# Kernel optimization log

Hardware: AMD Instinct MI355X
Metric: run time of the kernel (lower is better)

Reference implementation:

```python
import jax, jax.numpy as jnp
import numpy as np

D_MODEL = 1024
N_HEADS = 16
HEAD_DIM = D_MODEL // N_HEADS
N_EXPERTS = 4
HIDDEN = 4 * D_MODEL
B, T = 1, 2048


def _apply_rope(x, sin, cos):
    # x: [..., D]; sin/cos broadcastable to [..., D/2]
    x1, x2 = x[..., ::2], x[..., 1::2]
    r1 = x1 * cos - x2 * sin
    r2 = x1 * sin + x2 * cos
    return jnp.stack((r1, r2), axis=-1).reshape(x.shape)


def setup_inputs() -> dict:
    key = jax.random.key(0)
    ks = jax.random.split(key, 16)
    s = 0.02
    d, E, Hd = D_MODEL, N_EXPERTS, HIDDEN
    return {
        "x": jax.random.normal(ks[0], (B, T, d), dtype=jnp.float32),
        "w_dw": jax.random.normal(ks[1], (d, 3), dtype=jnp.float32) * s,      # depthwise conv k=3
        "w_pw": jax.random.normal(ks[2], (d, d), dtype=jnp.float32) * s,      # pointwise conv [out,in]
        "w_qkv": jax.random.normal(ks[3], (3 * d, d), dtype=jnp.float32) * s,  # [out,in]
        "w_o": jax.random.normal(ks[4], (d, d), dtype=jnp.float32) * s,
        "w_gate": jax.random.normal(ks[5], (d, d), dtype=jnp.float32) * s,
        "b_gate": jnp.zeros((d,), dtype=jnp.float32),
        "ln_g": jnp.ones((d,), dtype=jnp.float32),
        "ln_b": jnp.zeros((d,), dtype=jnp.float32),
        "w_moe_gate": jax.random.normal(ks[6], (E, d), dtype=jnp.float32) * s,  # Linear no bias [out,in]
        "w1": jax.random.normal(ks[7], (E, Hd, d), dtype=jnp.float32) * s,
        "b1": jnp.zeros((E, Hd), dtype=jnp.float32),
        "w2": jax.random.normal(ks[8], (E, d, Hd), dtype=jnp.float32) * s,
        "b2": jnp.zeros((E, d), dtype=jnp.float32),
    }


def reference(x, w_dw, w_pw, w_qkv, w_o, w_gate, b_gate, ln_g, ln_b,
              w_moe_gate, w1, b1, w2, b2):
    Bv, Tv, d = x.shape
    H, Dh = N_HEADS, HEAD_DIM
    dt = x.dtype

    # --- causal conv mixer (depthwise k=3, causal left pad 2, then pointwise) ---
    xp = jnp.pad(x, ((0, 0), (2, 0), (0, 0)))
    y = (xp[:, 0:Tv] * w_dw[:, 0] + xp[:, 1:Tv + 1] * w_dw[:, 1]
         + xp[:, 2:Tv + 2] * w_dw[:, 2])
    y = jnp.einsum('btd,ed->bte', y, w_pw)
    x = x + y

    # --- qkv projection + split heads ---
    qkv = jnp.einsum('btd,ed->bte', x, w_qkv).reshape(Bv, Tv, 3, H, Dh)
    q, k, v = qkv[:, :, 0], qkv[:, :, 1], qkv[:, :, 2]

    # --- RoPE (head_dim even) ---
    inv_freq = 1.0 / (10000.0 ** (jnp.arange(0, Dh, 2, dtype=dt) / Dh))
    pos = jnp.arange(Tv, dtype=dt)
    theta = pos[:, None] * inv_freq[None, :]                 # [T, Dh/2]
    sin = jnp.sin(theta)[None, :, None, :]                   # [1,T,1,Dh/2]
    cos = jnp.cos(theta)[None, :, None, :]
    q = _apply_rope(q, sin, cos)
    k = _apply_rope(k, sin, cos)

    # --- linear attention via full kv outer-product cumsum ---
    q_phi = jax.nn.elu(q) + 1.0
    k_phi = jax.nn.elu(k) + 1.0
    kv = k_phi[..., :, None] * v[..., None, :]               # [B,T,H,D,D]
    kv_prefix = jnp.cumsum(kv, axis=1)
    k_prefix = jnp.cumsum(k_phi, axis=1)
    num = jnp.einsum('bthd,bthdm->bthm', q_phi, kv_prefix)
    denom = jnp.sum(q_phi * k_prefix, axis=-1, keepdims=True)
    attn = num / (denom + 1e-6)
    attn = attn.reshape(Bv, Tv, d)
    attn = jnp.einsum('btd,ed->bte', attn, w_o)

    # --- delta-gated residual (dropout = identity in eval) ---
    delta = x - jnp.concatenate([x[:, :1], x[:, :-1]], axis=1)
    gate = jax.nn.sigmoid(jnp.einsum('btd,ed->bte', delta, w_gate) + b_gate)
    x = x + gate * attn

    # --- LayerNorm + dense MoE FFN ---
    mu = jnp.mean(x, axis=-1, keepdims=True)
    var = jnp.mean((x - mu) ** 2, axis=-1, keepdims=True)
    h = (x - mu) / jnp.sqrt(var + 1e-5) * ln_g + ln_b

    gw = jax.nn.softmax(jnp.einsum('btd,ed->bte', h, w_moe_gate), axis=-1)  # [B,T,E]
    hid = jax.nn.silu(jnp.einsum('btd,efd->btef', h, w1) + b1)              # [B,T,E,Hd]
    eo = jnp.einsum('btef,edf->bted', hid, w2) + b2                          # [B,T,E,d]
    ffn = jnp.einsum('bte,bted->btd', gw, eo)
    return x + ffn
```

## Files before the change

### kernel.cpp

```cpp
#include <hip/hip_runtime.h>
#include <hip/hip_bf16.h>

#define TSEQ 2048
#define DM   1024
#define NHD  16
#define DHD  64
#define NEXP 4
#define HIDN 4096
#define NMOE (NEXP*HIDN)
#define CHK  128
#define NCHK (TSEQ/CHK)

typedef __attribute__((ext_vector_type(8))) short          bf16x8_v;
typedef __attribute__((ext_vector_type(4))) float          f32x4_v;
typedef __attribute__((ext_vector_type(4))) unsigned short us4_v;

__device__ __forceinline__ unsigned short bfbits(float f) {
  __hip_bfloat16 h = __float2bfloat16(f);
  return __builtin_bit_cast(unsigned short, h);
}
__device__ __forceinline__ float bf2f(unsigned short u) {
  return __uint_as_float(((unsigned)u) << 16);
}
__device__ __forceinline__ float wave_sum(float v) {
  #pragma unroll
  for (int o = 32; o; o >>= 1) v += __shfl_xor(v, o, 64);
  return v;
}
__device__ __forceinline__ void gl_lds16(const void* g, void* l) {
  __builtin_amdgcn_global_load_lds((const __attribute__((address_space(1))) void*)g,
                                   (__attribute__((address_space(3))) void*)l, 16, 0, 0);
}

__global__ __launch_bounds__(256) void cvt_bf16(const float* __restrict__ in,
                                                unsigned short* __restrict__ out, int n4) {
  int i = blockIdx.x * 256 + threadIdx.x;
  if (i >= n4) return;
  float4 v = ((const float4*)in)[i];
  us4_v o; o.x = bfbits(v.x); o.y = bfbits(v.y); o.z = bfbits(v.z); o.w = bfbits(v.w);
  ((us4_v*)out)[i] = o;
}

__global__ __launch_bounds__(256) void perm_w2(const float* __restrict__ in,
                                               unsigned short* __restrict__ out) {
  int i = blockIdx.x * 256 + threadIdx.x;
  int i4 = i * 4;
  int f = i4 & (HIDN - 1);
  int r = i4 >> 12;
  int e = r >> 10, dd = r & 1023;
  float4 v = *(const float4*)&in[(size_t)r * HIDN + f];
  us4_v o; o.x = bfbits(v.x); o.y = bfbits(v.y); o.z = bfbits(v.z); o.w = bfbits(v.w);
  *(us4_v*)&out[(size_t)dd * NMOE + e * HIDN + f] = o;
}

__global__ __launch_bounds__(256) void conv_dw(const float* __restrict__ x,
                                               const float* __restrict__ w_dw,
                                               unsigned short* __restrict__ y_bf) {
  int i = blockIdx.x * 256 + threadIdx.x;
  int c = i & (DM - 1);
  int t = i >> 10;
  float a = (t >= 2) ? x[i - 2 * DM] : 0.f;
  float b = (t >= 1) ? x[i - DM]     : 0.f;
  float d = x[i];
  float y = a * w_dw[c * 3] + b * w_dw[c * 3 + 1] + d * w_dw[c * 3 + 2];
  y_bf[i] = bfbits(y);
}

template <int EPI>
__global__ __launch_bounds__(256) void gemm_bt(
    const unsigned short* __restrict__ A,  const unsigned short* __restrict__ A2,
    const unsigned short* __restrict__ B,  const unsigned short* __restrict__ B2,
    float* __restrict__ Cf, float* __restrict__ Cf2,
    unsigned short* __restrict__ Cbf,
    const float* __restrict__ ex0,
    int lda, int ldb, int K, int ldc)
{
  if (EPI == 0) { if (blockIdx.z) { A = A2; B = B2; Cf = Cf2; } }

  __shared__ unsigned short As[2][128][32];
  __shared__ unsigned short Bs[2][128][32];

  const int tid = threadIdx.x;
  const int m0 = blockIdx.x << 7, n0 = blockIdx.y << 7;
  const int sr = tid >> 2, sc = (tid & 3) << 3;
  const unsigned short* gA = A + (size_t)(m0 + sr) * lda + sc;
  const unsigned short* gB = B + (size_t)(n0 + sr) * ldb + sc;

  const int lane = tid & 63, wv = tid >> 6;
  const int wr = (wv >> 1) << 6, wc = (wv & 1) << 6;
  const int fr = lane & 15, fk = (lane >> 4) << 3, r4 = (lane >> 4) << 2;

  f32x4_v acc[4][4] = {};

  auto stage = [&](int k0, int b) {
    gl_lds16(gA + k0,                     &As[b][sr][sc]);
    gl_lds16(gA + k0 + (size_t)64 * lda,  &As[b][sr + 64][sc]);
    gl_lds16(gB + k0,                     &Bs[b][sr][sc]);
    gl_lds16(gB + k0 + (size_t)64 * ldb,  &Bs[b][sr + 64][sc]);
  };

  stage(0, 0);
  __syncthreads();
  int cur = 0;
  for (int k0 = 0; k0 < K; k0 += 32) {
    if (k0 + 32 < K) stage(k0 + 32, cur ^ 1);
    bf16x8_v af[4], bfm[4];
    #pragma unroll
    for (int m = 0; m < 4; m++) af[m]  = *(const bf16x8_v*)&As[cur][wr + m * 16 + fr][fk];
    #pragma unroll
    for (int n = 0; n < 4; n++) bfm[n] = *(const bf16x8_v*)&Bs[cur][wc + n * 16 + fr][fk];
    #pragma unroll
    for (int m = 0; m < 4; m++)
      #pragma unroll
      for (int n = 0; n < 4; n++)
        acc[m][n] = __builtin_amdgcn_mfma_f32_16x16x32_bf16(af[m], bfm[n], acc[m][n], 0, 0, 0);
    __syncthreads();
    cur ^= 1;
  }

  #pragma unroll
  for (int m = 0; m < 4; m++) {
    #pragma unroll
    for (int n = 0; n < 4; n++) {
      #pragma unroll
      for (int j = 0; j < 4; j++) {
        int gr = m0 + wr + m * 16 + r4 + j;
        int gc = n0 + wc + n * 16 + fr;
        float v = acc[m][n][j];
        size_t off = (size_t)gr * ldc + gc;
        if (EPI == 0) {
          Cf[off] = v;
        } else {
          float s = v + ex0[off];
          Cf[off] = s; Cbf[off] = bfbits(s);
        }
      }
    }
  }
}

template <int EPI>
__global__ __launch_bounds__(512, 1) void gemm256(
    const unsigned short* __restrict__ A, const unsigned short* __restrict__ B,
    float* __restrict__ Cf, unsigned short* __restrict__ Cbf,
    const float* __restrict__ ex0, const float* __restrict__ ex1,
    int lda, int ldb, int K, int ldc, int kPerZ)
{
  if (EPI == 1) { int ko = blockIdx.z * kPerZ; A += ko; B += ko; K = kPerZ; }

  __shared__ unsigned short As[2][256][64];
  __shared__ unsigned short Bs[2][256][64];

  int bidl = blockIdx.y * gridDim.x + blockIdx.x;
  int chunk = (gridDim.x * gridDim.y) >> 3;
  int swz = (bidl & 7) * chunk + (bidl >> 3);
  int m0 = (swz & 7) << 8, n0 = (swz >> 3) << 8;

  const int tid = threadIdx.x;
  const int srow = tid >> 3;
  const int scol = (tid & 7) << 3;
  const int scsw = (((tid & 7) ^ ((tid >> 3) & 7)) << 3);
  const unsigned short* gA = A + (size_t)(m0 + srow) * lda + scsw;
  const unsigned short* gB = B + (size_t)(n0 + srow) * ldb + scsw;

  auto stageA = [&](int k0, int b) {
    #pragma unroll
    for (int i = 0; i < 4; i++)
      gl_lds16(gA + (size_t)(i * 64) * lda + k0, &As[b][i * 64 + srow][scol]);
  };
  auto stageB = [&](int k0, int b) {
    #pragma unroll
    for (int i = 0; i < 4; i++)
      gl_lds16(gB + (size_t)(i * 64) * ldb + k0, &Bs[b][i * 64 + srow][scol]);
  };

  const int lane = tid & 63, wv = tid >> 6;
  const int wm = wv >> 2, wn = wv & 3;
  const int fr = lane & 15;
  const int kreg = lane >> 4, r4 = kreg << 2;
  const int c0 = ((kreg) ^ (lane & 7)) << 3;
  const int c1 = ((4 + kreg) ^ (lane & 7)) << 3;

  f32x4_v acc[8][4] = {};
  bf16x8_v a0[4][2], a1[4][2], bb[2][2];

  stageA(0, 0); stageB(0, 0);
  const int nt = K >> 6;
  for (int t = 0; t < nt; t++) {
    const int p = t & 1;
    if (t + 1 < nt) {
      stageA((t + 1) << 6, p ^ 1);
      asm volatile("s_waitcnt vmcnt(4)" ::: "memory");
    } else {
      asm volatile("s_waitcnt vmcnt(0)" ::: "memory");
    }
    __builtin_amdgcn_s_barrier();
    #pragma unroll
    for (int m = 0; m < 4; m++) {
      a0[m][0] = *(const bf16x8_v*)&As[p][wm * 128 + m * 16 + fr][c0];
      a0[m][1] = *(const bf16x8_v*)&As[p][wm * 128 + m * 16 + fr][c1];
    }
    #pragma unroll
    for (int n = 0; n < 2; n++) {
      bb[n][0] = *(const bf16x8_v*)&Bs[p][wn * 64 + n * 16 + fr][c0];
      bb[n][1] = *(const bf16x8_v*)&Bs[p][wn * 64 + n * 16 + fr][c1];
    }
    __builtin_amdgcn_s_setprio(1);
    #pragma unroll
    for (int m = 0; m < 4; m++)
      #pragma unroll
      for (int n = 0; n < 2; n++) {
        acc[m][n] = __builtin_amdgcn_mfma_f32_16x16x32_bf16(a0[m][0], bb[n][0], acc[m][n], 0, 0, 0);
        acc[m][n] = __builtin_amdgcn_mfma_f32_16x16x32_bf16(a0[m][1], bb[n][1], acc[m][n], 0, 0, 0);
      }
    __builtin_amdgcn_s_setprio(0);
    __builtin_amdgcn_s_barrier();
    #pragma unroll
    for (int m = 0; m < 4; m++) {
      a1[m][0] = *(const bf16x8_v*)&As[p][wm * 128 + 64 + m * 16 + fr][c0];
      a1[m][1] = *(const bf16x8_v*)&As[p][wm * 128 + 64 + m * 16 + fr][c1];
    }
    __builtin_amdgcn_s_setprio(1);
    #pragma unroll
    for (int m = 0; m < 4; m++)
      #pragma unroll
      for (int n = 0; n < 2; n++) {
        acc[m + 4][n] = __builtin_amdgcn_mfma_f32_16x16x32_bf16(a1[m][0], bb[n][0], acc[m + 4][n], 0, 0, 0);
        acc[m + 4][n] = __builtin_amdgcn_mfma_f32_16x16x32_bf16(a1[m][1], bb[n][1], acc[m + 4][n], 0, 0, 0);
      }
    __builtin_amdgcn_s_setprio(0);
    __builtin_amdgcn_s_barrier();
    #pragma unroll
    for (int n = 0; n < 2; n++) {
      bb[n][0] = *(const bf16x8_v*)&Bs[p][wn * 64 + 32 + n * 16 + fr][c0];
      bb[n][1] = *(const bf16x8_v*)&Bs[p][wn * 64 + 32 + n * 16 + fr][c1];
    }
    if (t + 1 < nt) stageB((t + 1) << 6, p ^ 1);
    __builtin_amdgcn_s_setprio(1);
    #pragma unroll
    for (int m = 0; m < 4; m++)
      #pragma unroll
      for (int n = 0; n < 2; n++) {
        acc[m][n + 2] = __builtin_amdgcn_mfma_f32_16x16x32_bf16(a0[m][0], bb[n][0], acc[m][n + 2], 0, 0, 0);
        acc[m][n + 2] = __builtin_amdgcn_mfma_f32_16x16x32_bf16(a0[m][1], bb[n][1], acc[m][n + 2], 0, 0, 0);
      }
    __builtin_amdgcn_s_setprio(0);
    __builtin_amdgcn_s_barrier();
    __builtin_amdgcn_s_setprio(1);
    #pragma unroll
    for (int m = 0; m < 4; m++)
      #pragma unroll
      for (int n = 0; n < 2; n++) {
        acc[m + 4][n + 2] = __builtin_amdgcn_mfma_f32_16x16x32_bf16(a1[m][0], bb[n][0], acc[m + 4][n + 2], 0, 0, 0);
        acc[m + 4][n + 2] = __builtin_amdgcn_mfma_f32_16x16x32_bf16(a1[m][1], bb[n][1], acc[m + 4][n + 2], 0, 0, 0);
      }
    __builtin_amdgcn_s_setprio(0);
    __builtin_amdgcn_s_barrier();
  }

  #pragma unroll
  for (int m = 0; m < 8; m++)
    #pragma unroll
    for (int n = 0; n < 4; n++)
      #pragma unroll
      for (int j = 0; j < 4; j++) {
        int grow = m0 + wm * 128 + m * 16 + r4 + j;
        int gcol = n0 + wn * 64 + n * 16 + fr;
        size_t off = (size_t)grow * ldc + gcol;
        if (EPI == 0) {
          float c2 = acc[m][n][j] + ex0[gcol];
          float sl = c2 / (1.f + __expf(-c2));
          Cbf[off] = bfbits(sl * ex1[grow * 4 + (gcol >> 12)]);
        } else {
          atomicAdd(&Cf[off], acc[m][n][j]);
        }
      }
}

__global__ __launch_bounds__(256) void rope_phi(const float* __restrict__ qkv,
                                                unsigned short* __restrict__ qphi,
                                                unsigned short* __restrict__ kphi,
                                                unsigned short* __restrict__ vout) {
  int idx = blockIdx.x * 256 + threadIdx.x;
  int i = idx & 31;
  int h = (idx >> 5) & 15;
  int t = idx >> 9;
  const float* row = qkv + (size_t)t * 3 * DM;
  int col = h * 64 + 2 * i;
  float q0 = row[col],          q1 = row[col + 1];
  float k0 = row[DM + col],     k1 = row[DM + col + 1];
  float v0 = row[2 * DM + col], v1 = row[2 * DM + col + 1];
  float invf = __expf(-(float)(2 * i) * (9.210340371976184f / 64.f));
  float th = (float)t * invf;
  float s, c;
  sincosf(th, &s, &c);
  float qr0 = q0 * c - q1 * s, qr1 = q0 * s + q1 * c;
  float kr0 = k0 * c - k1 * s, kr1 = k0 * s + k1 * c;
  size_t o = (size_t)t * DM + col;
  qphi[o]     = bfbits(qr0 > 0.f ? qr0 + 1.f : __expf(qr0));
  qphi[o + 1] = bfbits(qr1 > 0.f ? qr1 + 1.f : __expf(qr1));
  kphi[o]     = bfbits(kr0 > 0.f ? kr0 + 1.f : __expf(kr0));
  kphi[o + 1] = bfbits(kr1 > 0.f ? kr1 + 1.f : __expf(kr1));
  vout[o]     = bfbits(v0);
  vout[o + 1] = bfbits(v1);
}

__global__ __launch_bounds__(256) void kv_chunk(const unsigned short* __restrict__ kphi,
                                                const unsigned short* __restrict__ vbf,
                                                float* __restrict__ kvT,
                                                float* __restrict__ ksbuf) {
  int h = blockIdx.x & 15, c = blockIdx.x >> 4;
  __shared__ unsigned short Kt[64][136];
  __shared__ unsigned short Vt[64][136];
  int tid = threadIdx.x;
  int rr = tid >> 3, cc = (tid & 7) << 3;
  int t0 = c * CHK;
  #pragma unroll
  for (int g = 0; g < 4; g++) {
    int t = g * 32 + rr;
    bf16x8_v k8 = *(const bf16x8_v*)&kphi[(size_t)(t0 + t) * DM + h * 64 + cc];
    bf16x8_v v8 = *(const bf16x8_v*)&vbf [(size_t)(t0 + t) * DM + h * 64 + cc];
    #pragma unroll
    for (int j = 0; j < 8; j++) { Kt[cc + j][t] = (unsigned short)k8[j];
                                  Vt[cc + j][t] = (unsigned short)v8[j]; }
  }
  __syncthreads();
  int lane = tid & 63, wv = tid >> 6;
  int wr = (wv >> 1) << 5, wc = (wv & 1) << 5;
  int fr = lane & 15, fk = (lane >> 4) << 3, r4 = (lane >> 4) << 2;
  f32x4_v acc[2][2] = {};
  #pragma unroll
  for (int k0 = 0; k0 < 128; k0 += 32) {
    bf16x8_v a[2], b[2];
    #pragma unroll
    for (int m = 0; m < 2; m++) a[m] = *(const bf16x8_v*)&Kt[wr + m * 16 + fr][k0 + fk];
    #pragma unroll
    for (int n = 0; n < 2; n++) b[n] = *(const bf16x8_v*)&Vt[wc + n * 16 + fr][k0 + fk];
    #pragma unroll
    for (int m = 0; m < 2; m++)
      #pragma unroll
      for (int n = 0; n < 2; n++)
        acc[m][n] = __builtin_amdgcn_mfma_f32_16x16x32_bf16(a[m], b[n], acc[m][n], 0, 0, 0);
  }
  float* kvout = kvT + (size_t)(h * NCHK + c) * 4096;
  #pragma unroll
  for (int m = 0; m < 2; m++)
    #pragma unroll
    for (int n = 0; n < 2; n++)
      #pragma unroll
      for (int j = 0; j < 4; j++)
        kvout[(wc + n * 16 + fr) * 64 + (wr + m * 16 + r4 + j)] = acc[m][n][j];
  float s = 0.f;
  int d = tid >> 2, q = tid & 3;
  for (int i = 0; i < 32; i++) s += bf2f(Kt[d][q * 32 + i]);
  s += __shfl_xor(s, 1, 64); s += __shfl_xor(s, 2, 64);
  if (q == 0) ksbuf[(h * NCHK + c) * 64 + d] = s;
}

__global__ __launch_bounds__(256) void prefix_kv(const float* __restrict__ kvT,
                                                 const float* __restrict__ ksbuf,
                                                 unsigned short* __restrict__ sT,
                                                 float* __restrict__ kspre) {
  int idx = blockIdx.x * 256 + threadIdx.x;
  int h = idx >> 12, nd = idx & 4095;
  float s = 0.f;
  for (int c = 0; c < NCHK; c++) {
    size_t o = (size_t)(h * NCHK + c) * 4096 + nd;
    sT[o] = bfbits(s);
    s += kvT[o];
  }
  if (idx < NHD * 64) {
    float ks = 0.f;
    for (int c = 0; c < NCHK; c++) {
      int o = ((idx >> 6) * NCHK + c) * 64 + (idx & 63);
      kspre[o] = ks;
      ks += ksbuf[o];
    }
  }
}

__global__ __launch_bounds__(256) void attn_chunk(const unsigned short* __restrict__ qphi,
                                                  const unsigned short* __restrict__ kphi,
                                                  const unsigned short* __restrict__ vbf,
                                                  const unsigned short* __restrict__ sT,
                                                  const float* __restrict__ kspre,
                                                  float* __restrict__ num,
                                                  float* __restrict__ den) {
  int h = blockIdx.x & 15, c = blockIdx.x >> 4;
  __shared__ unsigned short Qs[128][72];
  __shared__ unsigned short Ks[128][72];
  __shared__ unsigned short Ms[128][200];
  __shared__ unsigned short Vt[64][200];
  __shared__ float ksL[64];
  int tid = threadIdx.x;
  int t0 = c * CHK;
  int rr = tid >> 3, cc = (tid & 7) << 3;
  #pragma unroll
  for (int g = 0; g < 4; g++) {
    int t = g * 32 + rr;
    bf16x8_v q8 = *(const bf16x8_v*)&qphi[(size_t)(t0 + t) * DM + h * 64 + cc];
    bf16x8_v k8 = *(const bf16x8_v*)&kphi[(size_t)(t0 + t) * DM + h * 64 + cc];
    bf16x8_v v8 = *(const bf16x8_v*)&vbf [(size_t)(t0 + t) * DM + h * 64 + cc];
    *(bf16x8_v*)&Qs[t][cc] = q8;
    *(bf16x8_v*)&Ks[t][cc] = k8;
    *(bf16x8_v*)&Ms[t][128 + cc] = q8;
    #pragma unroll
    for (int j = 0; j < 8; j++) Vt[cc + j][t] = (unsigned short)v8[j];
  }
  #pragma unroll
  for (int g = 0; g < 2; g++) {
    int e = (g * 256 + tid) * 8;
    bf16x8_v s8 = *(const bf16x8_v*)&sT[(size_t)(h * NCHK + c) * 4096 + e];
    *(bf16x8_v*)&Vt[e >> 6][128 + (e & 63)] = s8;
  }
  if (tid < 64) ksL[tid] = kspre[(h * NCHK + c) * 64 + tid];
  __syncthreads();

  int lane = tid & 63, wv = tid >> 6;
  int wr = (wv >> 1) << 6, wc = (wv & 1) << 6;
  int fr = lane & 15, fk = (lane >> 4) << 3, r4 = (lane >> 4) << 2;
  {
    f32x4_v acc[4][4] = {};
    #pragma unroll
    for (int k0 = 0; k0 < 64; k0 += 32) {
      bf16x8_v a[4], b[4];
      #pragma unroll
      for (int m = 0; m < 4; m++) a[m] = *(const bf16x8_v*)&Qs[wr + m * 16 + fr][k0 + fk];
      #pragma unroll
      for (int n = 0; n < 4; n++) b[n] = *(const bf16x8_v*)&Ks[wc + n * 16 + fr][k0 + fk];
      #pragma unroll
      for (int m = 0; m < 4; m++)
        #pragma unroll
        for (int n = 0; n < 4; n++)
          acc[m][n] = __builtin_amdgcn_mfma_f32_16x16x32_bf16(a[m], b[n], acc[m][n], 0, 0, 0);
    }
    #pragma unroll
    for (int m = 0; m < 4; m++)
      #pragma unroll
      for (int n = 0; n < 4; n++)
        #pragma unroll
        for (int j = 0; j < 4; j++) {
          int r = wr + m * 16 + r4 + j, col = wc + n * 16 + fr;
          Ms[r][col] = bfbits(col <= r ? acc[m][n][j] : 0.f);
        }
  }
  __syncthreads();
  {
    int dr = tid >> 1, half = tid & 1;
    float s = 0.f;
    for (int i = 0; i < 64; i++) s += bf2f(Ms[dr][half * 64 + i]);
    for (int i = 0; i < 32; i++) {
      int d = half * 32 + i;
      s += bf2f(Qs[dr][d]) * ksL[d];
    }
    s += __shfl_xor(s, 1, 64);
    if (!half) den[(size_t)(t0 + dr) * NHD + h] = s;
  }
  {
    int wc2 = (wv & 1) << 5;
    f32x4_v acc[4][2] = {};
    #pragma unroll
    for (int k0 = 0; k0 < 192; k0 += 32) {
      bf16x8_v a[4], b[2];
      #pragma unroll
      for (int m = 0; m < 4; m++) a[m] = *(const bf16x8_v*)&Ms[wr + m * 16 + fr][k0 + fk];
      #pragma unroll
      for (int n = 0; n < 2; n++) b[n] = *(const bf16x8_v*)&Vt[wc2 + n * 16 + fr][k0 + fk];
      #pragma unroll
      for (int m = 0; m < 4; m++)
        #pragma unroll
        for (int n = 0; n < 2; n++)
          acc[m][n] = __builtin_amdgcn_mfma_f32_16x16x32_bf16(a[m], b[n], acc[m][n], 0, 0, 0);
    }
    #pragma unroll
    for (int m = 0; m < 4; m++)
      #pragma unroll
      for (int n = 0; n < 2; n++)
        #pragma unroll
        for (int j = 0; j < 4; j++)
          num[(size_t)(t0 + wr + m * 16 + r4 + j) * DM + h * 64 + wc2 + n * 16 + fr]
              = acc[m][n][j];
  }
}

__global__ __launch_bounds__(256) void div_cvt(const float* __restrict__ attn_num,
                                               const float* __restrict__ denom,
                                               const float* __restrict__ x1,
                                               unsigned short* __restrict__ attn_bf,
                                               unsigned short* __restrict__ delta_bf) {
  int i = blockIdx.x * 256 + threadIdx.x;
  int i4 = i * 4;
  int t = i4 >> 10, c = i4 & 1023, h = c >> 6;
  float dn = 1.f / (denom[t * NHD + h] + 1e-6f);
  float4 nm = *(const float4*)&attn_num[i4];
  us4_v a; a.x = bfbits(nm.x * dn); a.y = bfbits(nm.y * dn);
           a.z = bfbits(nm.z * dn); a.w = bfbits(nm.w * dn);
  *(us4_v*)&attn_bf[i4] = a;
  float4 xv = *(const float4*)&x1[i4];
  float4 xp = t ? *(const float4*)&x1[i4 - DM] : xv;
  us4_v d; d.x = bfbits(xv.x - xp.x); d.y = bfbits(xv.y - xp.y);
           d.z = bfbits(xv.z - xp.z); d.w = bfbits(xv.w - xp.w);
  *(us4_v*)&delta_bf[i4] = d;
}

__global__ __launch_bounds__(256) void fuse_ln(const float* __restrict__ x1,
                                               const float* __restrict__ attn_o,
                                               const float* __restrict__ gate_lin,
                                               const float* __restrict__ b_gate,
                                               const float* __restrict__ ln_g,
                                               const float* __restrict__ ln_b,
                                               const float* __restrict__ w_moe,
                                               float* __restrict__ x2,
                                               unsigned short* __restrict__ h_bf,
                                               float* __restrict__ gw) {
  int t = blockIdx.x;
  int tid = threadIdx.x;
  __shared__ float hrow[DM];
  __shared__ float red[16];
  float vals[4], s = 0.f, s2 = 0.f;
  #pragma unroll
  for (int j = 0; j < 4; j++) {
    int c = tid + j * 256;
    size_t ix = (size_t)t * DM + c;
    float g = gate_lin[ix] + b_gate[c];
    float sig = 1.f / (1.f + __expf(-g));
    float xv = x1[ix] + sig * attn_o[ix];
    x2[ix] = xv; vals[j] = xv; s += xv; s2 += xv * xv;
  }
  s = wave_sum(s); s2 = wave_sum(s2);
  int wvi = tid >> 6, l = tid & 63;
  if (l == 0) { red[wvi] = s; red[4 + wvi] = s2; }
  __syncthreads();
  s  = red[0] + red[1] + red[2] + red[3];
  s2 = red[4] + red[5] + red[6] + red[7];
  float mu = s * (1.f / DM);
  float var = s2 * (1.f / DM) - mu * mu;
  float rstd = rsqrtf(var + 1e-5f);
  #pragma unroll
  for (int j = 0; j < 4; j++) {
    int c = tid + j * 256;
    size_t ix = (size_t)t * DM + c;
    float h = (vals[j] - mu) * rstd * ln_g[c] + ln_b[c];
    h_bf[ix] = bfbits(h); hrow[c] = h;
  }
  __syncthreads();
  float dot = 0.f;
  for (int i0 = l; i0 < DM; i0 += 64) dot += hrow[i0] * w_moe[wvi * DM + i0];
  dot = wave_sum(dot);
  if (l == 0) red[8 + wvi] = dot;
  __syncthreads();
  if (tid == 0) {
    float a0 = red[8], a1 = red[9], a2 = red[10], a3 = red[11];
    float mx = fmaxf(fmaxf(a0, a1), fmaxf(a2, a3));
    float e0 = __expf(a0 - mx), e1 = __expf(a1 - mx), e2 = __expf(a2 - mx), e3 = __expf(a3 - mx);
    float inv = 1.f / (e0 + e1 + e2 + e3);
    gw[t * 4 + 0] = e0 * inv; gw[t * 4 + 1] = e1 * inv;
    gw[t * 4 + 2] = e2 * inv; gw[t * 4 + 3] = e3 * inv;
  }
}

__global__ __launch_bounds__(256) void init_out(const float* __restrict__ x2,
                                                const float* __restrict__ gw,
                                                const float* __restrict__ b2,
                                                float* __restrict__ out) {
  int i = blockIdx.x * 256 + threadIdx.x;
  int i4 = i * 4;
  int t = i4 >> 10, c = i4 & 1023;
  const float* g = gw + t * 4;
  float4 o = *(const float4*)&x2[i4];
  #pragma unroll
  for (int e = 0; e < 4; e++) {
    float ge = g[e];
    float4 b = *(const float4*)&b2[e * DM + c];
    o.x += ge * b.x; o.y += ge * b.y; o.z += ge * b.z; o.w += ge * b.w;
  }
  *(float4*)&out[i4] = o;
}

extern "C" void kernel_launch(void* const* d_in, const int* in_sizes, int n_in,
                              void* d_out, int out_size, void* d_ws, size_t ws_size,
                              hipStream_t stream) {
  const float* x      = (const float*)d_in[0];
  const float* w_dw   = (const float*)d_in[1];
  const float* w_pw   = (const float*)d_in[2];
  const float* w_qkv  = (const float*)d_in[3];
  const float* w_o    = (const float*)d_in[4];
  const float* w_gate = (const float*)d_in[5];
  const float* b_gate = (const float*)d_in[6];
  const float* ln_g   = (const float*)d_in[7];
  const float* ln_b   = (const float*)d_in[8];
  const float* w_moe  = (const float*)d_in[9];
  const float* w1     = (const float*)d_in[10];
  const float* b1     = (const float*)d_in[11];
  const float* w2     = (const float*)d_in[12];
  const float* b2     = (const float*)d_in[13];
  float* out = (float*)d_out;

  char* ws = (char*)d_ws;
  size_t off = 0;
  auto alloc = [&](size_t bytes) -> char* {
    char* p = ws + off; off += (bytes + 255) & ~(size_t)255; return p;
  };
  unsigned short* w_pw_bf   = (unsigned short*)alloc((size_t)DM * DM * 2);
  unsigned short* w_qkv_bf  = (unsigned short*)alloc((size_t)3 * DM * DM * 2);
  unsigned short* w_o_bf    = (unsigned short*)alloc((size_t)DM * DM * 2);
  unsigned short* w_gate_bf = (unsigned short*)alloc((size_t)DM * DM * 2);
  unsigned short* w1_bf     = (unsigned short*)alloc((size_t)NMOE * DM * 2);
  unsigned short* w2c_bf    = (unsigned short*)alloc((size_t)DM * NMOE * 2);
  float*          x1        = (float*)alloc((size_t)TSEQ * DM * 4);
  unsigned short* x1_bf     = (unsigned short*)alloc((size_t)TSEQ * DM * 2);
  unsigned short* y_bf      = (unsigned short*)alloc((size_t)TSEQ * DM * 2);
  float*          denomb    = (float*)alloc((size_t)TSEQ * NHD * 4);
  float*          gwb       = (float*)alloc((size_t)TSEQ * NEXP * 4);
  float*          attn_o    = (float*)alloc((size_t)TSEQ * DM * 4);
  unsigned short* delta_bf  = (unsigned short*)alloc((size_t)TSEQ * DM * 2);
  float*          gate_lin  = (float*)alloc((size_t)TSEQ * DM * 4);
  float*          x2        = (float*)alloc((size_t)TSEQ * DM * 4);
  unsigned short* h_bf      = (unsigned short*)alloc((size_t)TSEQ * DM * 2);
  float*          kvT       = (float*)alloc((size_t)NHD * NCHK * 4096 * 4);
  unsigned short* sTb       = (unsigned short*)alloc((size_t)NHD * NCHK * 4096 * 2);
  float*          ksbuf     = (float*)alloc((size_t)NHD * NCHK * 64 * 4);
  float*          kspre     = (float*)alloc((size_t)NHD * NCHK * 64 * 4);
  char*           pool      = alloc((size_t)TSEQ * NMOE * 2);
  if (off > ws_size) return;

  float*          qkv      = (float*)pool;
  unsigned short* qphi     = (unsigned short*)(pool + (size_t)TSEQ * 3 * DM * 4);
  unsigned short* kphi     = qphi + (size_t)TSEQ * DM;
  unsigned short* vbf      = kphi + (size_t)TSEQ * DM;
  float*          attn_num = (float*)(vbf + (size_t)TSEQ * DM);
  unsigned short* attn_bf  = (unsigned short*)(attn_num + (size_t)TSEQ * DM);
  unsigned short* hids     = (unsigned short*)pool;

  cvt_bf16<<<1024,  256, 0, stream>>>(w_pw,   w_pw_bf,   DM * DM / 4);
  cvt_bf16<<<3072,  256, 0, stream>>>(w_qkv,  w_qkv_bf,  3 * DM * DM / 4);
  cvt_bf16<<<1024,  256, 0, stream>>>(w_o,    w_o_bf,    DM * DM / 4);
  cvt_bf16<<<1024,  256, 0, stream>>>(w_gate, w_gate_bf, DM * DM / 4);
  cvt_bf16<<<16384, 256, 0, stream>>>(w1,     w1_bf,     NMOE * DM / 4);
  perm_w2<<<16384, 256, 0, stream>>>(w2, w2c_bf);

  conv_dw<<<8192, 256, 0, stream>>>(x, w_dw, y_bf);
  gemm_bt<1><<<dim3(16, 8, 1), 256, 0, stream>>>(y_bf, nullptr, w_pw_bf, nullptr,
      x1, nullptr, x1_bf, x, DM, DM, DM, DM);

  gemm_bt<0><<<dim3(16, 24, 1), 256, 0, stream>>>(x1_bf, nullptr, w_qkv_bf, nullptr,
      qkv, nullptr, nullptr, nullptr, DM, DM, DM, 3 * DM);
  rope_phi<<<4096, 256, 0, stream>>>(qkv, qphi, kphi, vbf);

  kv_chunk<<<NHD * NCHK, 256, 0, stream>>>(kphi, vbf, kvT, ksbuf);
  prefix_kv<<<256, 256, 0, stream>>>(kvT, ksbuf, sTb, kspre);
  attn_chunk<<<NHD * NCHK, 256, 0, stream>>>(qphi, kphi, vbf, sTb, kspre,
                                             attn_num, denomb);
  div_cvt<<<2048, 256, 0, stream>>>(attn_num, denomb, x1, attn_bf, delta_bf);

  gemm_bt<0><<<dim3(16, 8, 2), 256, 0, stream>>>(attn_bf, delta_bf, w_o_bf, w_gate_bf,
      attn_o, gate_lin, nullptr, nullptr, DM, DM, DM, DM);

  fuse_ln<<<2048, 256, 0, stream>>>(x1, attn_o, gate_lin, b_gate, ln_g, ln_b, w_moe,
                                    x2, h_bf, gwb);

  init_out<<<2048, 256, 0, stream>>>(x2, gwb, b2, out);
  gemm256<0><<<dim3(8, 64, 1), 512, 0, stream>>>(h_bf, w1_bf, nullptr, hids,
      b1, gwb, DM, DM, DM, NMOE, 0);
  gemm256<1><<<dim3(8, 4, 8), 512, 0, stream>>>(hids, w2c_bf, out, nullptr,
      nullptr, nullptr, NMOE, NMOE, NMOE, DM, NMOE / 8);
}
```

Measured before the change: 387.9 us.

## Rework small GEMMs, fuse attention normalization, drop w2 permute, trim barriers

```diff
diff --git a/kernel.cpp b/kernel.cpp
--- a/kernel.cpp
+++ b/kernel.cpp
@@ -39,18 +39,6 @@
   float4 v = ((const float4*)in)[i];
   us4_v o; o.x = bfbits(v.x); o.y = bfbits(v.y); o.z = bfbits(v.z); o.w = bfbits(v.w);
   ((us4_v*)out)[i] = o;
-}
-
-__global__ __launch_bounds__(256) void perm_w2(const float* __restrict__ in,
-                                               unsigned short* __restrict__ out) {
-  int i = blockIdx.x * 256 + threadIdx.x;
-  int i4 = i * 4;
-  int f = i4 & (HIDN - 1);
-  int r = i4 >> 12;
-  int e = r >> 10, dd = r & 1023;
-  float4 v = *(const float4*)&in[(size_t)r * HIDN + f];
-  us4_v o; o.x = bfbits(v.x); o.y = bfbits(v.y); o.z = bfbits(v.z); o.w = bfbits(v.w);
-  *(us4_v*)&out[(size_t)dd * NMOE + e * HIDN + f] = o;
 }
 
 __global__ __launch_bounds__(256) void conv_dw(const float* __restrict__ x,
@@ -67,76 +55,102 @@
 }
 
 template <int EPI>
-__global__ __launch_bounds__(256) void gemm_bt(
-    const unsigned short* __restrict__ A,  const unsigned short* __restrict__ A2,
-    const unsigned short* __restrict__ B,  const unsigned short* __restrict__ B2,
+__global__ __launch_bounds__(256, 2) void gemm128s(
+    const unsigned short* __restrict__ A, const unsigned short* __restrict__ A2,
+    const unsigned short* __restrict__ B, const unsigned short* __restrict__ B2,
     float* __restrict__ Cf, float* __restrict__ Cf2,
-    unsigned short* __restrict__ Cbf,
-    const float* __restrict__ ex0,
+    unsigned short* __restrict__ Cbf, const float* __restrict__ ex0,
     int lda, int ldb, int K, int ldc)
 {
   if (EPI == 0) { if (blockIdx.z) { A = A2; B = B2; Cf = Cf2; } }
 
-  __shared__ unsigned short As[2][128][32];
-  __shared__ unsigned short Bs[2][128][32];
+  __shared__ unsigned short As[2][128][64];
+  __shared__ unsigned short Bs[2][128][64];
+
+  const int nwg = gridDim.x * gridDim.y;
+  const int bidl = blockIdx.y * gridDim.x + blockIdx.x;
+  const int chunk = nwg >> 3;
+  const int swz = (bidl & 7) * chunk + (bidl >> 3);
+  const int ntn = gridDim.y;
+  const int rest = swz >> 3;
+  const int m0 = ((rest / ntn) * 8 + (swz & 7)) << 7;
+  const int n0 = (rest % ntn) << 7;
 
   const int tid = threadIdx.x;
-  const int m0 = blockIdx.x << 7, n0 = blockIdx.y << 7;
-  const int sr = tid >> 2, sc = (tid & 3) << 3;
-  const unsigned short* gA = A + (size_t)(m0 + sr) * lda + sc;
-  const unsigned short* gB = B + (size_t)(n0 + sr) * ldb + sc;
+  const int srow = tid >> 3;
+  const int scol = (tid & 7) << 3;
+  const int scsw = (((tid & 7) ^ ((tid >> 3) & 7)) << 3);
+  const unsigned short* gA = A + (size_t)(m0 + srow) * lda + scsw;
+  const unsigned short* gB = B + (size_t)(n0 + srow) * ldb + scsw;
+
+  auto stage = [&](int k0, int b) {
+    #pragma unroll
+    for (int i = 0; i < 4; i++)
+      gl_lds16(gA + (size_t)(i * 32) * lda + k0, &As[b][i * 32 + srow][scol]);
+    #pragma unroll
+    for (int i = 0; i < 4; i++)
+      gl_lds16(gB + (size_t)(i * 32) * ldb + k0, &Bs[b][i * 32 + srow][scol]);
+  };
 
   const int lane = tid & 63, wv = tid >> 6;
   const int wr = (wv >> 1) << 6, wc = (wv & 1) << 6;
-  const int fr = lane & 15, fk = (lane >> 4) << 3, r4 = (lane >> 4) << 2;
+  const int fr = lane & 15, kreg = lane >> 4, r4 = kreg << 2;
+  const int c0 = ((kreg) ^ (lane & 7)) << 3;
+  const int c1 = ((4 + kreg) ^ (lane & 7)) << 3;
 
   f32x4_v acc[4][4] = {};
 
-  auto stage = [&](int k0, int b) {
-    gl_lds16(gA + k0,                     &As[b][sr][sc]);
-    gl_lds16(gA + k0 + (size_t)64 * lda,  &As[b][sr + 64][sc]);
-    gl_lds16(gB + k0,                     &Bs[b][sr][sc]);
-    gl_lds16(gB + k0 + (size_t)64 * ldb,  &Bs[b][sr + 64][sc]);
-  };
-
   stage(0, 0);
-  __syncthreads();
-  int cur = 0;
-  for (int k0 = 0; k0 < K; k0 += 32) {
-    if (k0 + 32 < K) stage(k0 + 32, cur ^ 1);
-    bf16x8_v af[4], bfm[4];
-    #pragma unroll
-    for (int m = 0; m < 4; m++) af[m]  = *(const bf16x8_v*)&As[cur][wr + m * 16 + fr][fk];
-    #pragma unroll
-    for (int n = 0; n < 4; n++) bfm[n] = *(const bf16x8_v*)&Bs[cur][wc + n * 16 + fr][fk];
+  const int nt = K >> 6;
+  for (int t = 0; t < nt; t++) {
+    const int p = t & 1;
+    if (t + 1 < nt) {
+      stage((t + 1) << 6, p ^ 1);
+      asm volatile("s_waitcnt vmcnt(8)" ::: "memory");
+    } else {
+      asm volatile("s_waitcnt vmcnt(0)" ::: "memory");
+    }
+    __builtin_amdgcn_s_barrier();
+    __builtin_amdgcn_sched_barrier(0);
+    bf16x8_v af[4][2], bfm[4][2];
+    #pragma unroll
+    for (int m = 0; m < 4; m++) {
+      af[m][0] = *(const bf16x8_v*)&As[p][wr + m * 16 + fr][c0];
+      af[m][1] = *(const bf16x8_v*)&As[p][wr + m * 16 + fr][c1];
+    }
+    #pragma unroll
+    for (int n = 0; n < 4; n++) {
+      bfm[n][0] = *(const bf16x8_v*)&Bs[p][wc + n * 16 + fr][c0];
+      bfm[n][1] = *(const bf16x8_v*)&Bs[p][wc + n * 16 + fr][c1];
+    }
+    __builtin_amdgcn_s_setprio(1);
     #pragma unroll
     for (int m = 0; m < 4; m++)
       #pragma unroll
-      for (int n = 0; n < 4; n++)
-        acc[m][n] = __builtin_amdgcn_mfma_f32_16x16x32_bf16(af[m], bfm[n], acc[m][n], 0, 0, 0);
-    __syncthreads();
-    cur ^= 1;
-  }
-
-  #pragma unroll
-  for (int m = 0; m < 4; m++) {
-    #pragma unroll
-    for (int n = 0; n < 4; n++) {
+      for (int n = 0; n < 4; n++) {
+        acc[m][n] = __builtin_amdgcn_mfma_f32_16x16x32_bf16(af[m][0], bfm[n][0], acc[m][n], 0, 0, 0);
+        acc[m][n] = __builtin_amdgcn_mfma_f32_16x16x32_bf16(af[m][1], bfm[n][1], acc[m][n], 0, 0, 0);
+      }
+    __builtin_amdgcn_s_setprio(0);
+    __builtin_amdgcn_s_barrier();
+  }
+
+  #pragma unroll
+  for (int m = 0; m < 4; m++)
+    #pragma unroll
+    for (int n = 0; n < 4; n++)
       #pragma unroll
       for (int j = 0; j < 4; j++) {
-        int gr = m0 + wr + m * 16 + r4 + j;
-        int gc = n0 + wc + n * 16 + fr;
-        float v = acc[m][n][j];
-        size_t off = (size_t)gr * ldc + gc;
+        int grow = m0 + wr + m * 16 + r4 + j;
+        int gcol = n0 + wc + n * 16 + fr;
+        size_t off = (size_t)grow * ldc + gcol;
         if (EPI == 0) {
-          Cf[off] = v;
+          Cf[off] = acc[m][n][j];
         } else {
-          float s = v + ex0[off];
+          float s = acc[m][n][j] + ex0[off];
           Cf[off] = s; Cbf[off] = bfbits(s);
         }
       }
-    }
-  }
 }
 
 template <int EPI>
@@ -146,7 +160,12 @@
     const float* __restrict__ ex0, const float* __restrict__ ex1,
     int lda, int ldb, int K, int ldc, int kPerZ)
 {
-  if (EPI == 1) { int ko = blockIdx.z * kPerZ; A += ko; B += ko; K = kPerZ; }
+  if (EPI == 1) {
+    int ko = blockIdx.z * kPerZ;
+    A += ko;
+    B += (size_t)(ko >> 12) * DM * HIDN + (ko & 4095);
+    K = kPerZ;
+  }
 
   __shared__ unsigned short As[2][256][64];
   __shared__ unsigned short Bs[2][256][64];
@@ -195,6 +214,7 @@
       asm volatile("s_waitcnt vmcnt(0)" ::: "memory");
     }
     __builtin_amdgcn_s_barrier();
+    __builtin_amdgcn_sched_barrier(0);
     #pragma unroll
     for (int m = 0; m < 4; m++) {
       a0[m][0] = *(const bf16x8_v*)&As[p][wm * 128 + m * 16 + fr][c0];
@@ -214,7 +234,6 @@
         acc[m][n] = __builtin_amdgcn_mfma_f32_16x16x32_bf16(a0[m][1], bb[n][1], acc[m][n], 0, 0, 0);
       }
     __builtin_amdgcn_s_setprio(0);
-    __builtin_amdgcn_s_barrier();
     #pragma unroll
     for (int m = 0; m < 4; m++) {
       a1[m][0] = *(const bf16x8_v*)&As[p][wm * 128 + 64 + m * 16 + fr][c0];
@@ -229,7 +248,6 @@
         acc[m + 4][n] = __builtin_amdgcn_mfma_f32_16x16x32_bf16(a1[m][1], bb[n][1], acc[m + 4][n], 0, 0, 0);
       }
     __builtin_amdgcn_s_setprio(0);
-    __builtin_amdgcn_s_barrier();
     #pragma unroll
     for (int n = 0; n < 2; n++) {
       bb[n][0] = *(const bf16x8_v*)&Bs[p][wn * 64 + 32 + n * 16 + fr][c0];
@@ -244,9 +262,6 @@
         acc[m][n + 2] = __builtin_amdgcn_mfma_f32_16x16x32_bf16(a0[m][0], bb[n][0], acc[m][n + 2], 0, 0, 0);
         acc[m][n + 2] = __builtin_amdgcn_mfma_f32_16x16x32_bf16(a0[m][1], bb[n][1], acc[m][n + 2], 0, 0, 0);
       }
-    __builtin_amdgcn_s_setprio(0);
-    __builtin_amdgcn_s_barrier();
-    __builtin_amdgcn_s_setprio(1);
     #pragma unroll
     for (int m = 0; m < 4; m++)
       #pragma unroll
@@ -384,14 +399,14 @@
                                                   const unsigned short* __restrict__ vbf,
                                                   const unsigned short* __restrict__ sT,
                                                   const float* __restrict__ kspre,
-                                                  float* __restrict__ num,
-                                                  float* __restrict__ den) {
+                                                  unsigned short* __restrict__ attn_bf) {
   int h = blockIdx.x & 15, c = blockIdx.x >> 4;
   __shared__ unsigned short Qs[128][72];
   __shared__ unsigned short Ks[128][72];
   __shared__ unsigned short Ms[128][200];
   __shared__ unsigned short Vt[64][200];
   __shared__ float ksL[64];
+  __shared__ float denL[128];
   int tid = threadIdx.x;
   int t0 = c * CHK;
   int rr = tid >> 3, cc = (tid & 7) << 3;
@@ -454,8 +469,9 @@
       s += bf2f(Qs[dr][d]) * ksL[d];
     }
     s += __shfl_xor(s, 1, 64);
-    if (!half) den[(size_t)(t0 + dr) * NHD + h] = s;
-  }
+    if (!half) denL[dr] = 1.f / (s + 1e-6f);
+  }
+  __syncthreads();
   {
     int wc2 = (wv & 1) << 5;
     f32x4_v acc[4][2] = {};
@@ -477,30 +493,26 @@
       #pragma unroll
       for (int n = 0; n < 2; n++)
         #pragma unroll
-        for (int j = 0; j < 4; j++)
-          num[(size_t)(t0 + wr + m * 16 + r4 + j) * DM + h * 64 + wc2 + n * 16 + fr]
-              = acc[m][n][j];
-  }
-}
-
-__global__ __launch_bounds__(256) void div_cvt(const float* __restrict__ attn_num,
-                                               const float* __restrict__ denom,
-                                               const float* __restrict__ x1,
-                                               unsigned short* __restrict__ attn_bf,
-                                               unsigned short* __restrict__ delta_bf) {
+        for (int j = 0; j < 4; j++) {
+          int row = wr + m * 16 + r4 + j;
+          attn_bf[(size_t)(t0 + row) * DM + h * 64 + wc2 + n * 16 + fr]
+              = bfbits(acc[m][n][j] * denL[row]);
+        }
+  }
+}
+
+__global__ __launch_bounds__(256) void delta_cvt(const unsigned short* __restrict__ x1b,
+                                                 unsigned short* __restrict__ delta_bf) {
   int i = blockIdx.x * 256 + threadIdx.x;
-  int i4 = i * 4;
-  int t = i4 >> 10, c = i4 & 1023, h = c >> 6;
-  float dn = 1.f / (denom[t * NHD + h] + 1e-6f);
-  float4 nm = *(const float4*)&attn_num[i4];
-  us4_v a; a.x = bfbits(nm.x * dn); a.y = bfbits(nm.y * dn);
-           a.z = bfbits(nm.z * dn); a.w = bfbits(nm.w * dn);
-  *(us4_v*)&attn_bf[i4] = a;
-  float4 xv = *(const float4*)&x1[i4];
-  float4 xp = t ? *(const float4*)&x1[i4 - DM] : xv;
-  us4_v d; d.x = bfbits(xv.x - xp.x); d.y = bfbits(xv.y - xp.y);
-           d.z = bfbits(xv.z - xp.z); d.w = bfbits(xv.w - xp.w);
-  *(us4_v*)&delta_bf[i4] = d;
+  int i8 = i * 8;
+  int t = i8 >> 10;
+  bf16x8_v cur = *(const bf16x8_v*)&x1b[i8];
+  bf16x8_v prv = t ? *(const bf16x8_v*)&x1b[i8 - DM] : cur;
+  bf16x8_v o;
+  #pragma unroll
+  for (int j = 0; j < 8; j++)
+    o[j] = (short)bfbits(bf2f((unsigned short)cur[j]) - bf2f((unsigned short)prv[j]));
+  *(bf16x8_v*)&delta_bf[i8] = o;
 }
 
 __global__ __launch_bounds__(256) void fuse_ln(const float* __restrict__ x1,
@@ -606,11 +618,10 @@
   unsigned short* w_o_bf    = (unsigned short*)alloc((size_t)DM * DM * 2);
   unsigned short* w_gate_bf = (unsigned short*)alloc((size_t)DM * DM * 2);
   unsigned short* w1_bf     = (unsigned short*)alloc((size_t)NMOE * DM * 2);
-  unsigned short* w2c_bf    = (unsigned short*)alloc((size_t)DM * NMOE * 2);
+  unsigned short* w2_bf     = (unsigned short*)alloc((size_t)NEXP * DM * HIDN * 2);
   float*          x1        = (float*)alloc((size_t)TSEQ * DM * 4);
   unsigned short* x1_bf     = (unsigned short*)alloc((size_t)TSEQ * DM * 2);
   unsigned short* y_bf      = (unsigned short*)alloc((size_t)TSEQ * DM * 2);
-  float*          denomb    = (float*)alloc((size_t)TSEQ * NHD * 4);
   float*          gwb       = (float*)alloc((size_t)TSEQ * NEXP * 4);
   float*          attn_o    = (float*)alloc((size_t)TSEQ * DM * 4);
   unsigned short* delta_bf  = (unsigned short*)alloc((size_t)TSEQ * DM * 2);
@@ -628,8 +639,7 @@
   unsigned short* qphi     = (unsigned short*)(pool + (size_t)TSEQ * 3 * DM * 4);
   unsigned short* kphi     = qphi + (size_t)TSEQ * DM;
   unsigned short* vbf      = kphi + (size_t)TSEQ * DM;
-  float*          attn_num = (float*)(vbf + (size_t)TSEQ * DM);
-  unsigned short* attn_bf  = (unsigned short*)(attn_num + (size_t)TSEQ * DM);
+  unsigned short* attn_bf  = vbf + (size_t)TSEQ * DM;
   unsigned short* hids     = (unsigned short*)pool;
 
   cvt_bf16<<<1024,  256, 0, stream>>>(w_pw,   w_pw_bf,   DM * DM / 4);
@@ -637,23 +647,22 @@
   cvt_bf16<<<1024,  256, 0, stream>>>(w_o,    w_o_bf,    DM * DM / 4);
   cvt_bf16<<<1024,  256, 0, stream>>>(w_gate, w_gate_bf, DM * DM / 4);
   cvt_bf16<<<16384, 256, 0, stream>>>(w1,     w1_bf,     NMOE * DM / 4);
-  perm_w2<<<16384, 256, 0, stream>>>(w2, w2c_bf);
+  cvt_bf16<<<16384, 256, 0, stream>>>(w2,     w2_bf,     NEXP * DM * HIDN / 4);
 
   conv_dw<<<8192, 256, 0, stream>>>(x, w_dw, y_bf);
-  gemm_bt<1><<<dim3(16, 8, 1), 256, 0, stream>>>(y_bf, nullptr, w_pw_bf, nullptr,
+  gemm128s<1><<<dim3(16, 8, 1), 256, 0, stream>>>(y_bf, nullptr, w_pw_bf, nullptr,
       x1, nullptr, x1_bf, x, DM, DM, DM, DM);
 
-  gemm_bt<0><<<dim3(16, 24, 1), 256, 0, stream>>>(x1_bf, nullptr, w_qkv_bf, nullptr,
+  gemm128s<0><<<dim3(16, 24, 1), 256, 0, stream>>>(x1_bf, nullptr, w_qkv_bf, nullptr,
       qkv, nullptr, nullptr, nullptr, DM, DM, DM, 3 * DM);
   rope_phi<<<4096, 256, 0, stream>>>(qkv, qphi, kphi, vbf);
 
   kv_chunk<<<NHD * NCHK, 256, 0, stream>>>(kphi, vbf, kvT, ksbuf);
   prefix_kv<<<256, 256, 0, stream>>>(kvT, ksbuf, sTb, kspre);
-  attn_chunk<<<NHD * NCHK, 256, 0, stream>>>(qphi, kphi, vbf, sTb, kspre,
-                                             attn_num, denomb);
-  div_cvt<<<2048, 256, 0, stream>>>(attn_num, denomb, x1, attn_bf, delta_bf);
-
-  gemm_bt<0><<<dim3(16, 8, 2), 256, 0, stream>>>(attn_bf, delta_bf, w_o_bf, w_gate_bf,
+  attn_chunk<<<NHD * NCHK, 256, 0, stream>>>(qphi, kphi, vbf, sTb, kspre, attn_bf);
+  delta_cvt<<<1024, 256, 0, stream>>>(x1_bf, delta_bf);
+
+  gemm128s<0><<<dim3(16, 8, 2), 256, 0, stream>>>(attn_bf, delta_bf, w_o_bf, w_gate_bf,
       attn_o, gate_lin, nullptr, nullptr, DM, DM, DM, DM);
 
   fuse_ln<<<2048, 256, 0, stream>>>(x1, attn_o, gate_lin, b_gate, ln_g, ln_b, w_moe,
@@ -662,6 +671,6 @@
   init_out<<<2048, 256, 0, stream>>>(x2, gwb, b2, out);
   gemm256<0><<<dim3(8, 64, 1), 512, 0, stream>>>(h_bf, w1_bf, nullptr, hids,
       b1, gwb, DM, DM, DM, NMOE, 0);
-  gemm256<1><<<dim3(8, 4, 8), 512, 0, stream>>>(hids, w2c_bf, out, nullptr,
-      nullptr, nullptr, NMOE, NMOE, NMOE, DM, NMOE / 8);
-}
+  gemm256<1><<<dim3(8, 4, 8), 512, 0, stream>>>(hids, w2_bf, out, nullptr,
+      nullptr, nullptr, NMOE, HIDN, NMOE, DM, NMOE / 8);
+}
```

After: 366.2 us. 1.06x faster.
